# Kernel optimization log

Hardware: AMD Instinct MI355X
Metric: run time of the kernel (lower is better)

The kernel has to match this reference:

```python
import jax, jax.numpy as jnp
import numpy as np

B, L, N, H, HU = 512, 16, 10000, 128, 128

def _rn(k, shape, s=0.05):
    return jax.random.normal(k, shape, jnp.float32) * s

def setup_inputs():
    ks = jax.random.split(jax.random.key(0), 26)
    return dict(
        x=jax.random.normal(ks[0], (B, 2), jnp.float32),
        t0_res=jax.random.normal(ks[1], (B, 1), jnp.float32),
        node_inputs=jax.random.normal(ks[2], (B, 2 * L, N), jnp.float32),
        tau_inputs=jax.random.normal(ks[3], (B, L, 1), jnp.float32),
        end=jax.random.normal(ks[4], (B, 2), jnp.float32),
        coords=jax.random.normal(ks[5], (B, 2 * L, 2), jnp.float32),
        Wx1=_rn(ks[6], (1, 2)), Wx2=_rn(ks[7], (H, 1)), bx2=_rn(ks[8], (H,)),
        Wres=_rn(ks[9], (H, 1)), bres=_rn(ks[10], (H,)),
        Wnode=_rn(ks[11], (H, N)),
        Wtau=_rn(ks[12], (H, 1)), btau=_rn(ks[13], (H,)),
        Wend1=_rn(ks[14], (1, 2)), Wend2=_rn(ks[15], (H, 1)), bend2=_rn(ks[16], (H,)),
        Wcoord=_rn(ks[17], (H, 2)),
        lstm_Wih=_rn(ks[18], (7, 4 * H, H)), lstm_Whh=_rn(ks[19], (7, 4 * H, H)),
        lstm_bih=_rn(ks[20], (7, 4 * H)), lstm_bhh=_rn(ks[21], (7, 4 * H)),
        head_W1=_rn(ks[22], (7, HU, H)), head_b1=_rn(ks[23], (7, HU)),
        head_W2=_rn(ks[24], (7, 1, HU)), head_b2=_rn(ks[25], (7, 1)),
    )

def _lstm_last(s, Wih, Whh, bih, bhh):
    # s: [T, B, H] (time-first, like torch LSTM default). PyTorch gate order: i, f, g, o.
    h0 = jnp.zeros((s.shape[1], Whh.shape[1]), s.dtype)
    def step(carry, xt):
        h, c = carry
        g = xt @ Wih.T + h @ Whh.T + (bih + bhh)
        i, f, gg, o = jnp.split(g, 4, axis=-1)
        c = jax.nn.sigmoid(f) * c + jax.nn.sigmoid(i) * jnp.tanh(gg)
        h = jax.nn.sigmoid(o) * jnp.tanh(c)
        return (h, c), None
    (h, _), _ = jax.lax.scan(step, (h0, h0), s)
    return h  # last output == last hidden state

def _forward(x, t0_res, node_inputs, tau_inputs, end, coords,
             Wx1, Wx2, bx2, Wres, bres, Wnode, Wtau, btau,
             Wend1, Wend2, bend2, Wcoord,
             lstm_Wih, lstm_Whh, lstm_bih, lstm_bhh,
             head_W1, head_b1, head_W2, head_b2):
    xh = jnp.tanh((x @ Wx1.T) @ Wx2.T + bx2)        # [B,H]
    t0h = jnp.tanh(t0_res @ Wres.T + bres)          # [B,H]
    nodeh = node_inputs @ Wnode.T                   # [B,2L,H] (dominant memory-bound GEMM)
    tauh = jnp.tanh(tau_inputs @ Wtau.T + btau)     # [B,L,H]
    endh = (end @ Wend1.T) @ Wend2.T + bend2        # [B,H]
    coordh = coords @ Wcoord.T                      # [B,2L,H]
    ne, no = nodeh[:, 0::2], nodeh[:, 1::2]         # even/odd walk nodes [B,L,H]
    ce, co = coordh[:, 0::2], coordh[:, 1::2]
    def interleave(parts):  # k x [B,L,H] -> time-first [k*L, B, H], per-step order preserved
        s = jnp.stack(parts, axis=2)
        return jnp.swapaxes(s.reshape(s.shape[0], -1, s.shape[-1]), 0, 1)
    pre = jnp.stack([xh, t0h], axis=0)  # [2,B,H]
    suf = endh[None]                    # [1,B,H]
    seqs = [
        jnp.concatenate([pre, interleave([tauh, ne, ce, no, co]), suf], 0),  # all        T=5L+3
        jnp.concatenate([pre, interleave([tauh]), suf], 0),                  # time       T=L+3
        jnp.swapaxes(nodeh, 0, 1),                                           # node       T=2L
        jnp.swapaxes(coordh, 0, 1),                                          # coord      T=2L
        jnp.concatenate([pre, interleave([tauh, ne, no]), suf], 0),          # node_time  T=3L+3
        interleave([ne, ce, no, co]),                                        # node_coord T=4L
        jnp.concatenate([pre, interleave([tauh, ce, co]), suf], 0),          # time_coord T=3L+3
    ]
    outs = []
    for k, s in enumerate(seqs):
        h = _lstm_last(s, lstm_Wih[k], lstm_Whh[k], lstm_bih[k], lstm_bhh[k])
        outs.append(jnp.tanh(h @ head_W1[k].T + head_b1[k]) @ head_W2[k].T + head_b2[k])
    return tuple(outs)  # matches torch return order: all, time, node, coord, node_time, node_coord, time_coord

def reference(x, t0_res, node_inputs, tau_inputs, end, coords,
              Wx1, Wx2, bx2, Wres, bres, Wnode, Wtau, btau,
              Wend1, Wend2, bend2, Wcoord,
              lstm_Wih, lstm_Whh, lstm_bih, lstm_bhh,
              head_W1, head_b1, head_W2, head_b2):
    return _forward(x, t0_res, node_inputs, tau_inputs, end, coords,
                    Wx1, Wx2, bx2, Wres, bres, Wnode, Wtau, btau,
                    Wend1, Wend2, bend2, Wcoord,
                    lstm_Wih, lstm_Whh, lstm_bih, lstm_bhh,
                    head_W1, head_b1, head_W2, head_b2)
```

## Files before the change

kernel.cpp:

```cpp
#include <hip/hip_runtime.h>
#include <hip/hip_fp16.h>

typedef _Float16 f16;
typedef _Float16 f16x8 __attribute__((ext_vector_type(8)));
typedef float f32x4 __attribute__((ext_vector_type(4)));

#define NB 512
#define NL 16
#define NK 10000
#define NH 128
#define NSF 316
#define NT128 79

__device__ __forceinline__ float fast_exp2(float x) {
#if __has_builtin(__builtin_amdgcn_exp2f)
  return __builtin_amdgcn_exp2f(x);
#else
  return exp2f(x);
#endif
}
__device__ __forceinline__ float fast_rcp(float x) {
#if __has_builtin(__builtin_amdgcn_rcpf)
  return __builtin_amdgcn_rcpf(x);
#else
  return 1.f / x;
#endif
}
__device__ __forceinline__ float sigf(float x) {
  return fast_rcp(1.f + fast_exp2(-1.44269504f * x));
}
__device__ __forceinline__ float tanh_fast(float x) {
  return 2.f * fast_rcp(1.f + fast_exp2(-2.88539008f * x)) - 1.f;
}

__device__ __forceinline__ void gload16(const void* g, void* l) {
  __builtin_amdgcn_global_load_lds(
      (const __attribute__((address_space(1))) unsigned int*)g,
      (__attribute__((address_space(3))) unsigned int*)l, 16, 0, 0);
}

__global__ void prep_kernel(
    const float* __restrict__ x, const float* __restrict__ t0,
    const float* __restrict__ tau, const float* __restrict__ endi,
    const float* __restrict__ coords,
    const float* __restrict__ Wx1, const float* __restrict__ Wx2,
    const float* __restrict__ bx2, const float* __restrict__ Wres,
    const float* __restrict__ bres, const float* __restrict__ Wnode,
    const float* __restrict__ Wtau, const float* __restrict__ btau,
    const float* __restrict__ Wend1, const float* __restrict__ Wend2,
    const float* __restrict__ bend2, const float* __restrict__ Wcoord,
    const float* __restrict__ Wih, const float* __restrict__ Whh,
    const float* __restrict__ bih, const float* __restrict__ bhh,
    f16* __restrict__ xh, f16* __restrict__ t0h, f16* __restrict__ endh,
    f16* __restrict__ tauh, f16* __restrict__ coordh, f16* __restrict__ Wf,
    f16* __restrict__ Wih16, f16* __restrict__ Whh16, float* __restrict__ bsum) {
  const int tid0 = blockIdx.x * blockDim.x + threadIdx.x;
  const int stride = gridDim.x * blockDim.x;

  const int nWf = NSF * 4096;
  const int nW = 7 * 512 * NH;
  const int nb = 7 * 512;
  const int nxh = NB * NH;
  const int ntau = NB * NL * NH;
  const int nco = NB * 2 * NL * NH;

  for (int i = tid0; i < nWf; i += stride) {
    const int s = i >> 12, r = i & 4095;
    const int nt = r >> 9, l2 = r & 511;
    const int lane = l2 >> 3, e = l2 & 7;
    const int kg = lane >> 4, lr = lane & 15;
    const int col = nt * 16 + lr;
    const int k = s * 32 + kg * 8 + e;
    Wf[i] = (k < NK) ? (f16)Wnode[(size_t)col * NK + k] : (f16)0.f;
  }
  for (int i = tid0; i < nW; i += stride) {
    Wih16[i] = (f16)Wih[i];
    Whh16[i] = (f16)Whh[i];
  }
  for (int i = tid0; i < nb; i += stride) bsum[i] = bih[i] + bhh[i];
  for (int i = tid0; i < nxh; i += stride) {
    const int b = i >> 7, h = i & 127;
    const float s = x[2 * b] * Wx1[0] + x[2 * b + 1] * Wx1[1];
    xh[i] = (f16)tanhf(s * Wx2[h] + bx2[h]);
    t0h[i] = (f16)tanhf(t0[b] * Wres[h] + bres[h]);
    const float e = endi[2 * b] * Wend1[0] + endi[2 * b + 1] * Wend1[1];
    endh[i] = (f16)(e * Wend2[h] + bend2[h]);
  }
  for (int i = tid0; i < ntau; i += stride) {
    const int h = i & 127, bl = i >> 7;
    tauh[i] = (f16)tanhf(tau[bl] * Wtau[h] + btau[h]);
  }
  for (int i = tid0; i < nco; i += stride) {
    const int h = i & 127, br = i >> 7;
    coordh[i] = (f16)(coords[2 * br] * Wcoord[2 * h] +
                      coords[2 * br + 1] * Wcoord[2 * h + 1]);
  }
}

__global__ __launch_bounds__(512, 2) void node_gemm(const float* __restrict__ A,
                                                    const f16* __restrict__ Wf,
                                                    f16* __restrict__ Cn) {
  __shared__ char lds[4][32768];
  const int tid = threadIdx.x;
  const int w = tid >> 6, l = tid & 63;
  const int lr = l & 15, kg = l >> 4;
  const int r0 = blockIdx.x * 64;
  char* lds0 = &lds[0][0];

  const char* ap[4];
  int bnd[4];
#pragma unroll
  for (int i = 0; i < 4; i++) {
    const int row = w * 8 + i * 2 + (l >> 5);
    const int bswz = ((l & 31) * 16) ^ ((row & 7) << 4);
    ap[i] = (const char*)A + (size_t)(r0 + row) * 40000 + bswz;
    bnd[i] = 39984 - bswz;
  }

  const int rs = w & 3;
  const int nt0 = (w >> 2) * 4;
  int rdoA[4][2];
#pragma unroll
  for (int ks = 0; ks < 4; ks++) {
    const int row = rs * 16 + lr;
    const int s = (row & 7) << 4;
#pragma unroll
    for (int h = 0; h < 2; h++)
      rdoA[ks][h] = row * 512 + ((ks * 128 + kg * 32 + h * 16) ^ s);
  }

  f32x4 acc[4];
#pragma unroll
  for (int j = 0; j < 4; j++) {
    f32x4 z = {0.f, 0.f, 0.f, 0.f};
    acc[j] = z;
  }

  auto burst = [&](int ta) {
    const int tb0 = ta * 512, tb1 = tb0 + 512;
    char* d0 = lds0 + (ta & 3) * 32768 + w * 4096;
    char* d1 = lds0 + ((ta + 1) & 3) * 32768 + w * 4096;
    const bool two = (ta + 1 < NT128);
#pragma unroll
    for (int i = 0; i < 4; i++) {
      gload16(ap[i] + (tb0 < bnd[i] ? tb0 : bnd[i]), d0 + i * 1024);
      if (two) gload16(ap[i] + (tb1 < bnd[i] ? tb1 : bnd[i]), d1 + i * 1024);
    }
  };

  auto loadB = [&](int t, f16x8 (&B)[4][4]) {
    const f16* bp = Wf + (size_t)(4 * t) * 4096 + nt0 * 512 + l * 8;
#pragma unroll
    for (int j = 0; j < 4; j++)
#pragma unroll
      for (int ks = 0; ks < 4; ks++)
        B[j][ks] = *(const f16x8*)(bp + (size_t)ks * 4096 + j * 512);
  };

  auto compute = [&](int buf, const f16x8 (&B)[4][4]) {
    const char* cb = lds0 + buf * 32768;
#pragma unroll
    for (int ks = 0; ks < 4; ks++) {
      const f32x4 a0 = *(const f32x4*)(cb + rdoA[ks][0]);
      const f32x4 a1 = *(const f32x4*)(cb + rdoA[ks][1]);
      f16x8 af;
      af[0] = (f16)a0[0]; af[1] = (f16)a0[1]; af[2] = (f16)a0[2]; af[3] = (f16)a0[3];
      af[4] = (f16)a1[0]; af[5] = (f16)a1[1]; af[6] = (f16)a1[2]; af[7] = (f16)a1[3];
#pragma unroll
      for (int j = 0; j < 4; j++)
        acc[j] = __builtin_amdgcn_mfma_f32_16x16x32_f16(af, B[j][ks], acc[j], 0, 0, 0);
    }
  };

  f16x8 BA[4][4], BB[4][4];

  burst(0);
  loadB(0, BA);

  for (int e = 0; e < NT128; e += 2) {
    asm volatile("s_waitcnt vmcnt(16)" ::: "memory");
    __builtin_amdgcn_s_barrier();
    if (e + 1 < NT128) loadB(e + 1, BB);
    if (e + 2 < NT128) burst(e + 2);
    compute(e & 3, BA);
    if (e + 1 < NT128) {
      if (e + 2 < NT128) loadB(e + 2, BA);
      compute((e + 1) & 3, BB);
    }
  }

  f16* crow = Cn + (size_t)(r0 + rs * 16 + kg * 4) * NH + nt0 * 16 + lr;
#pragma unroll
  for (int j = 0; j < 4; j++)
#pragma unroll
    for (int jr = 0; jr < 4; jr++)
      crow[(size_t)jr * NH + j * 16] = (f16)acc[j][jr];
}

__global__ __launch_bounds__(512, 2) void lstm_run(
    const f16* __restrict__ xh, const f16* __restrict__ t0h,
    const f16* __restrict__ endh, const f16* __restrict__ tauh,
    const f16* __restrict__ nodeh, const f16* __restrict__ coordh,
    const f16* __restrict__ Wih16, const f16* __restrict__ Whh16,
    const float* __restrict__ bsum, const float* __restrict__ hW1,
    const float* __restrict__ hb1, const float* __restrict__ hW2,
    const float* __restrict__ hb2, float* __restrict__ out) {
  __shared__ f16 hbuf[2][16 * NH];
  __shared__ float hu[16 * NH];

  const int k = blockIdx.x >> 5;
  const int b0 = (blockIdx.x & 31) << 4;
  const int w = threadIdx.x >> 6;
  const int l = threadIdx.x & 63;
  const int lr = l & 15, kg = l >> 4;

  int len;
  switch (k) {
    case 0: len = 83; break;
    case 1: len = 19; break;
    case 2: len = 32; break;
    case 3: len = 32; break;
    case 4: len = 51; break;
    case 5: len = 64; break;
    default: len = 51; break;
  }

  auto xptr = [&](int t) -> const f16* {
    const f16* cb; int bstr, idx;
    if (k == 2) { cb = nodeh; bstr = 32 * NH; idx = t; }
    else if (k == 3) { cb = coordh; bstr = 32 * NH; idx = t; }
    else if (k == 5) {
      const int q = t >> 2, r = t & 3;
      cb = (r == 0 || r == 2) ? nodeh : coordh;
      bstr = 32 * NH;
      idx = 2 * q + ((r >= 2) ? 1 : 0);
    } else {
      if (t == 0) { cb = xh; bstr = NH; idx = 0; }
      else if (t == 1) { cb = t0h; bstr = NH; idx = 0; }
      else if (t == len - 1) { cb = endh; bstr = NH; idx = 0; }
      else {
        const int u = t - 2;
        if (k == 0) {
          const int q = u / 5, r = u - 5 * q;
          if (r == 0) { cb = tauh; bstr = 16 * NH; idx = q; }
          else if (r == 1) { cb = nodeh; bstr = 32 * NH; idx = 2 * q; }
          else if (r == 2) { cb = coordh; bstr = 32 * NH; idx = 2 * q; }
          else if (r == 3) { cb = nodeh; bstr = 32 * NH; idx = 2 * q + 1; }
          else { cb = coordh; bstr = 32 * NH; idx = 2 * q + 1; }
        } else if (k == 1) { cb = tauh; bstr = 16 * NH; idx = u; }
        else if (k == 4) {
          const int q = u / 3, r = u - 3 * q;
          if (r == 0) { cb = tauh; bstr = 16 * NH; idx = q; }
          else { cb = nodeh; bstr = 32 * NH; idx = 2 * q + (r - 1); }
        } else {
          const int q = u / 3, r = u - 3 * q;
          if (r == 0) { cb = tauh; bstr = 16 * NH; idx = q; }
          else { cb = coordh; bstr = 32 * NH; idx = 2 * q + (r - 1); }
        }
      }
    }
    return cb + (size_t)(b0 + lr) * bstr + idx * NH + kg * 8;
  };

  f16x8 Wh[4][4], Wi[4][4];
  float bias[4];
  {
    const f16* whb = Whh16 + (size_t)k * 512 * NH;
    const f16* wib = Wih16 + (size_t)k * 512 * NH;
#pragma unroll
    for (int g = 0; g < 4; g++) {
      const int col = g * 128 + w * 16 + lr;
      bias[g] = bsum[k * 512 + col];
#pragma unroll
      for (int kc = 0; kc < 4; kc++) {
        Wh[kc][g] = *(const f16x8*)(whb + (size_t)col * NH + kc * 32 + kg * 8);
        Wi[kc][g] = *(const f16x8*)(wib + (size_t)col * NH + kc * 32 + kg * 8);
      }
    }
  }

  char* lds0 = (char*)&hbuf[0][0];
  *(unsigned long long*)(lds0 + threadIdx.x * 8) = 0ull;
  __syncthreads();

  float c[4] = {0, 0, 0, 0};

  int rdo[4];
#pragma unroll
  for (int kc = 0; kc < 4; kc++) {
    const int colb = (kc * 32 + kg * 8) * 2;
    rdo[kc] = lr * 256 + (colb ^ ((lr & 7) << 4));
  }
  int wro[4];
#pragma unroll
  for (int jr = 0; jr < 4; jr++) {
    const int hrow = kg * 4 + jr;
    const int hcol = w * 16 + lr;
    wro[jr] = hrow * 256 + ((hcol * 2) ^ ((hrow & 7) << 4));
  }

  f16x8 axc[4];
  {
    const f16* xp = xptr(0);
#pragma unroll
    for (int kc = 0; kc < 4; kc++) axc[kc] = *(const f16x8*)(xp + kc * 32);
  }

  int cur = 0;
  for (int t = 0; t < len; t++) {
    char* rb = lds0 + cur * 4096;
    f16x8 ah[4];
#pragma unroll
    for (int kc = 0; kc < 4; kc++) ah[kc] = *(const f16x8*)(rb + rdo[kc]);

    f16x8 axn[4];
    if (t + 1 < len) {
      const f16* xp = xptr(t + 1);
#pragma unroll
      for (int kc = 0; kc < 4; kc++) axn[kc] = *(const f16x8*)(xp + kc * 32);
    }

    f32x4 acc[4];
#pragma unroll
    for (int g = 0; g < 4; g++) {
      f32x4 binit = {bias[g], bias[g], bias[g], bias[g]};
      acc[g] = binit;
    }
#pragma unroll
    for (int kc = 0; kc < 4; kc++)
#pragma unroll
      for (int g = 0; g < 4; g++)
        acc[g] = __builtin_amdgcn_mfma_f32_16x16x32_f16(axc[kc], Wi[kc][g], acc[g], 0, 0, 0);
#pragma unroll
    for (int kc = 0; kc < 4; kc++)
#pragma unroll
      for (int g = 0; g < 4; g++)
        acc[g] = __builtin_amdgcn_mfma_f32_16x16x32_f16(ah[kc], Wh[kc][g], acc[g], 0, 0, 0);

    char* wb = lds0 + (cur ^ 1) * 4096;
#pragma unroll
    for (int jr = 0; jr < 4; jr++) {
      const float iv = acc[0][jr];
      const float fv = acc[1][jr];
      const float gv = acc[2][jr];
      const float ov = acc[3][jr];
      const float cn = sigf(fv) * c[jr] + sigf(iv) * tanh_fast(gv);
      c[jr] = cn;
      const float hn = sigf(ov) * tanh_fast(cn);
      *(f16*)(wb + wro[jr]) = (f16)hn;
    }
    __syncthreads();
#pragma unroll
    for (int kc = 0; kc < 4; kc++) axc[kc] = axn[kc];
    cur ^= 1;
  }

  {
    char* rb = lds0 + cur * 4096;
    f16x8 ah[4];
#pragma unroll
    for (int kc = 0; kc < 4; kc++) ah[kc] = *(const f16x8*)(rb + rdo[kc]);
    const float* W1 = hW1 + (size_t)k * NH * NH;
    const int col = w * 16 + lr;
    f32x4 hacc;
    {
      const float b1 = hb1[k * NH + col];
      f32x4 binit = {b1, b1, b1, b1};
      hacc = binit;
    }
#pragma unroll
    for (int kc = 0; kc < 4; kc++) {
      const float* wrow = W1 + (size_t)col * NH + kc * 32 + kg * 8;
      const f32x4 w0 = *(const f32x4*)(wrow);
      const f32x4 w1 = *(const f32x4*)(wrow + 4);
      f16x8 wv;
      wv[0] = (f16)w0[0]; wv[1] = (f16)w0[1]; wv[2] = (f16)w0[2]; wv[3] = (f16)w0[3];
      wv[4] = (f16)w1[0]; wv[5] = (f16)w1[1]; wv[6] = (f16)w1[2]; wv[7] = (f16)w1[3];
      hacc = __builtin_amdgcn_mfma_f32_16x16x32_f16(ah[kc], wv, hacc, 0, 0, 0);
    }
#pragma unroll
    for (int jr = 0; jr < 4; jr++)
      hu[(kg * 4 + jr) * NH + col] = tanh_fast(hacc[jr]);
  }
  __syncthreads();
  if (w == 0) {
    const int b = l >> 2, part = l & 3;
    const float* W2 = hW2 + (size_t)k * NH;
    float s = 0.f;
#pragma unroll
    for (int j = 0; j < 32; j++)
      s += hu[b * NH + part * 32 + j] * W2[part * 32 + j];
    s += __shfl_xor(s, 1);
    s += __shfl_xor(s, 2);
    if (part == 0) out[k * NB + b0 + b] = s + hb2[k];
  }
}

extern "C" void kernel_launch(void* const* d_in, const int* in_sizes, int n_in,
                              void* d_out, int out_size, void* d_ws, size_t ws_size,
                              hipStream_t stream) {
  (void)in_sizes; (void)n_in; (void)out_size; (void)ws_size;
  const float* x = (const float*)d_in[0];
  const float* t0 = (const float*)d_in[1];
  const float* node = (const float*)d_in[2];
  const float* tau = (const float*)d_in[3];
  const float* endi = (const float*)d_in[4];
  const float* coords = (const float*)d_in[5];
  const float* Wx1 = (const float*)d_in[6];
  const float* Wx2 = (const float*)d_in[7];
  const float* bx2 = (const float*)d_in[8];
  const float* Wres = (const float*)d_in[9];
  const float* bres = (const float*)d_in[10];
  const float* Wnode = (const float*)d_in[11];
  const float* Wtau = (const float*)d_in[12];
  const float* btau = (const float*)d_in[13];
  const float* Wend1 = (const float*)d_in[14];
  const float* Wend2 = (const float*)d_in[15];
  const float* bend2 = (const float*)d_in[16];
  const float* Wcoord = (const float*)d_in[17];
  const float* Wih = (const float*)d_in[18];
  const float* Whh = (const float*)d_in[19];
  const float* bih = (const float*)d_in[20];
  const float* bhh = (const float*)d_in[21];
  const float* hW1 = (const float*)d_in[22];
  const float* hb1 = (const float*)d_in[23];
  const float* hW2 = (const float*)d_in[24];
  const float* hb2 = (const float*)d_in[25];

  char* ws = (char*)d_ws;
  f16* xh = (f16*)ws;      ws += (size_t)NB * NH * 2;
  f16* t0h = (f16*)ws;     ws += (size_t)NB * NH * 2;
  f16* endh = (f16*)ws;    ws += (size_t)NB * NH * 2;
  f16* tauh = (f16*)ws;    ws += (size_t)NB * NL * NH * 2;
  f16* nodeh = (f16*)ws;   ws += (size_t)NB * 2 * NL * NH * 2;
  f16* coordh = (f16*)ws;  ws += (size_t)NB * 2 * NL * NH * 2;
  f16* Wf = (f16*)ws;      ws += (size_t)NSF * 4096 * 2;
  f16* Wih16 = (f16*)ws;   ws += (size_t)7 * 512 * NH * 2;
  f16* Whh16 = (f16*)ws;   ws += (size_t)7 * 512 * NH * 2;
  float* bsum = (float*)ws;

  prep_kernel<<<1024, 256, 0, stream>>>(
      x, t0, tau, endi, coords, Wx1, Wx2, bx2, Wres, bres, Wnode, Wtau, btau,
      Wend1, Wend2, bend2, Wcoord, Wih, Whh, bih, bhh,
      xh, t0h, endh, tauh, coordh, Wf, Wih16, Whh16, bsum);
  node_gemm<<<256, 512, 0, stream>>>(node, Wf, nodeh);
  lstm_run<<<224, 512, 0, stream>>>(xh, t0h, endh, tauh, nodeh, coordh,
                                    Wih16, Whh16, bsum, hW1, hb1, hW2, hb2,
                                    (float*)d_out);
}
```

Before: 299.3 us.

## Retile node GEMM warps to 64x32 split-K with LDS reduction

The node-projection GEMM changes its per-warp tile. Before, each warp covered 16 rows by 64 columns over the full K slice. Now each warp covers all 64 rows by 32 columns over half of each K tile, and the two K halves are summed through LDS at the end. This cuts per-warp weight (B) fragment loads from global memory by 4x and shrinks the B register buffers. In exchange, each warp does more LDS reads of A and more fp32-to-fp16 conversions, and an extra LDS reduction plus barrier is added. The vmcnt wait is retuned to the smaller load count and the last tile is peeled out of the loop.

```diff
diff --git a/kernel.cpp b/kernel.cpp
--- a/kernel.cpp
+++ b/kernel.cpp
@@ -117,24 +117,29 @@
     bnd[i] = 39984 - bswz;
   }
 
-  const int rs = w & 3;
-  const int nt0 = (w >> 2) * 4;
-  int rdoA[4][2];
-#pragma unroll
-  for (int ks = 0; ks < 4; ks++) {
-    const int row = rs * 16 + lr;
+  const int cp = w >> 1;
+  const int kw = w & 1;
+  int rdoA[4][2][2];
+#pragma unroll
+  for (int rg = 0; rg < 4; rg++) {
+    const int row = rg * 16 + lr;
     const int s = (row & 7) << 4;
 #pragma unroll
-    for (int h = 0; h < 2; h++)
-      rdoA[ks][h] = row * 512 + ((ks * 128 + kg * 32 + h * 16) ^ s);
-  }
-
-  f32x4 acc[4];
-#pragma unroll
-  for (int j = 0; j < 4; j++) {
-    f32x4 z = {0.f, 0.f, 0.f, 0.f};
-    acc[j] = z;
-  }
+    for (int ks = 0; ks < 2; ks++)
+#pragma unroll
+      for (int h = 0; h < 2; h++)
+        rdoA[rg][ks][h] =
+            row * 512 + ((kw * 256 + ks * 128 + kg * 32 + h * 16) ^ s);
+  }
+
+  f32x4 acc[4][2];
+#pragma unroll
+  for (int rg = 0; rg < 4; rg++)
+#pragma unroll
+    for (int j = 0; j < 2; j++) {
+      f32x4 z = {0.f, 0.f, 0.f, 0.f};
+      acc[rg][j] = z;
+    }
 
   auto burst = [&](int ta) {
     const int tb0 = ta * 512, tb1 = tb0 + 512;
@@ -148,53 +153,77 @@
     }
   };
 
-  auto loadB = [&](int t, f16x8 (&B)[4][4]) {
-    const f16* bp = Wf + (size_t)(4 * t) * 4096 + nt0 * 512 + l * 8;
-#pragma unroll
-    for (int j = 0; j < 4; j++)
-#pragma unroll
-      for (int ks = 0; ks < 4; ks++)
+  auto loadB = [&](int t, f16x8 (&B)[2][2]) {
+    const f16* bp = Wf + (size_t)(4 * t + 2 * kw) * 4096 + cp * 1024 + l * 8;
+#pragma unroll
+    for (int j = 0; j < 2; j++)
+#pragma unroll
+      for (int ks = 0; ks < 2; ks++)
         B[j][ks] = *(const f16x8*)(bp + (size_t)ks * 4096 + j * 512);
   };
 
-  auto compute = [&](int buf, const f16x8 (&B)[4][4]) {
-    const char* cb = lds0 + buf * 32768;
-#pragma unroll
-    for (int ks = 0; ks < 4; ks++) {
-      const f32x4 a0 = *(const f32x4*)(cb + rdoA[ks][0]);
-      const f32x4 a1 = *(const f32x4*)(cb + rdoA[ks][1]);
-      f16x8 af;
-      af[0] = (f16)a0[0]; af[1] = (f16)a0[1]; af[2] = (f16)a0[2]; af[3] = (f16)a0[3];
-      af[4] = (f16)a1[0]; af[5] = (f16)a1[1]; af[6] = (f16)a1[2]; af[7] = (f16)a1[3];
-#pragma unroll
-      for (int j = 0; j < 4; j++)
-        acc[j] = __builtin_amdgcn_mfma_f32_16x16x32_f16(af, B[j][ks], acc[j], 0, 0, 0);
-    }
+  auto compute = [&](int t, const f16x8 (&B)[2][2]) {
+    const char* cb = lds0 + (t & 3) * 32768;
+#pragma unroll
+    for (int ks = 0; ks < 2; ks++)
+#pragma unroll
+      for (int rg = 0; rg < 4; rg++) {
+        const f32x4 a0 = *(const f32x4*)(cb + rdoA[rg][ks][0]);
+        const f32x4 a1 = *(const f32x4*)(cb + rdoA[rg][ks][1]);
+        f16x8 af;
+        af[0] = (f16)a0[0]; af[1] = (f16)a0[1];
+        af[2] = (f16)a0[2]; af[3] = (f16)a0[3];
+        af[4] = (f16)a1[0]; af[5] = (f16)a1[1];
+        af[6] = (f16)a1[2]; af[7] = (f16)a1[3];
+#pragma unroll
+        for (int j = 0; j < 2; j++)
+          acc[rg][j] =
+              __builtin_amdgcn_mfma_f32_16x16x32_f16(af, B[j][ks], acc[rg][j], 0, 0, 0);
+      }
   };
 
-  f16x8 BA[4][4], BB[4][4];
+  f16x8 BA[2][2], BB[2][2];
 
   burst(0);
   loadB(0, BA);
 
-  for (int e = 0; e < NT128; e += 2) {
-    asm volatile("s_waitcnt vmcnt(16)" ::: "memory");
+  for (int e = 0; e < NT128 - 1; e += 2) {
+    asm volatile("s_waitcnt vmcnt(4)" ::: "memory");
     __builtin_amdgcn_s_barrier();
-    if (e + 1 < NT128) loadB(e + 1, BB);
-    if (e + 2 < NT128) burst(e + 2);
-    compute(e & 3, BA);
-    if (e + 1 < NT128) {
-      if (e + 2 < NT128) loadB(e + 2, BA);
-      compute((e + 1) & 3, BB);
-    }
-  }
-
-  f16* crow = Cn + (size_t)(r0 + rs * 16 + kg * 4) * NH + nt0 * 16 + lr;
-#pragma unroll
-  for (int j = 0; j < 4; j++)
-#pragma unroll
-    for (int jr = 0; jr < 4; jr++)
-      crow[(size_t)jr * NH + j * 16] = (f16)acc[j][jr];
+    loadB(e + 1, BB);
+    burst(e + 2);
+    compute(e, BA);
+    loadB(e + 2, BA);
+    compute(e + 1, BB);
+  }
+  asm volatile("s_waitcnt vmcnt(0)" ::: "memory");
+  __builtin_amdgcn_s_barrier();
+  compute(78, BA);
+
+  if (kw == 1) {
+#pragma unroll
+    for (int rg = 0; rg < 4; rg++)
+#pragma unroll
+      for (int j = 0; j < 2; j++) {
+        const int tl = (cp * 4 + rg) * 2 + j;
+        *(f32x4*)(lds0 + tl * 1024 + l * 16) = acc[rg][j];
+      }
+  }
+  __syncthreads();
+  if (kw == 0) {
+#pragma unroll
+    for (int rg = 0; rg < 4; rg++)
+#pragma unroll
+      for (int j = 0; j < 2; j++) {
+        const int tl = (cp * 4 + rg) * 2 + j;
+        const f32x4 p = *(const f32x4*)(lds0 + tl * 1024 + l * 16);
+        const f32x4 s = acc[rg][j] + p;
+        f16* crow =
+            Cn + (size_t)(r0 + rg * 16 + kg * 4) * NH + cp * 32 + j * 16 + lr;
+#pragma unroll
+        for (int jr = 0; jr < 4; jr++) crow[(size_t)jr * NH] = (f16)s[jr];
+      }
+  }
 }
 
 __global__ __launch_bounds__(512, 2) void lstm_run(
```

Result: faster. 266.9 us (-10.8%).

## Halve node GEMM row tile to 32 rows and double grid for more CTAs

Applied to the files above, without the earlier changes.

The node projection GEMM now gives each block 32 rows instead of 64, launching 512 blocks instead of 256. LDS per block halves and launch bounds allow four blocks per CU. Each wave now covers a 16x32 output slice instead of 16x64. The loop tail is peeled so the last tile is computed after a full wait, which removes the per-iteration bound checks. The aim is to fill all CUs (256 blocks underfilled the 256-CU part at two per CU) and keep more loads in flight. In exchange, each block re-reads the full weight matrix from global memory, doubling total B traffic.

```diff
diff --git a/kernel.cpp b/kernel.cpp
--- a/kernel.cpp
+++ b/kernel.cpp
@@ -97,101 +97,106 @@
   }
 }
 
-__global__ __launch_bounds__(512, 2) void node_gemm(const float* __restrict__ A,
+__global__ __launch_bounds__(512, 4) void node_gemm(const float* __restrict__ A,
                                                     const f16* __restrict__ Wf,
                                                     f16* __restrict__ Cn) {
-  __shared__ char lds[4][32768];
+  __shared__ char lds[4][16384];
   const int tid = threadIdx.x;
   const int w = tid >> 6, l = tid & 63;
   const int lr = l & 15, kg = l >> 4;
-  const int r0 = blockIdx.x * 64;
+  const int r0 = blockIdx.x * 32;
   char* lds0 = &lds[0][0];
 
-  const char* ap[4];
-  int bnd[4];
-#pragma unroll
-  for (int i = 0; i < 4; i++) {
-    const int row = w * 8 + i * 2 + (l >> 5);
+  const char* ap[2];
+  int bnd[2];
+#pragma unroll
+  for (int i = 0; i < 2; i++) {
+    const int row = w * 4 + i * 2 + (l >> 5);
     const int bswz = ((l & 31) * 16) ^ ((row & 7) << 4);
     ap[i] = (const char*)A + (size_t)(r0 + row) * 40000 + bswz;
     bnd[i] = 39984 - bswz;
   }
 
-  const int rs = w & 3;
-  const int nt0 = (w >> 2) * 4;
+  const int rh = w & 1;
+  const int cq = w >> 1;
   int rdoA[4][2];
-#pragma unroll
-  for (int ks = 0; ks < 4; ks++) {
-    const int row = rs * 16 + lr;
+  {
+    const int row = rh * 16 + lr;
     const int s = (row & 7) << 4;
 #pragma unroll
-    for (int h = 0; h < 2; h++)
-      rdoA[ks][h] = row * 512 + ((ks * 128 + kg * 32 + h * 16) ^ s);
-  }
-
-  f32x4 acc[4];
-#pragma unroll
-  for (int j = 0; j < 4; j++) {
+    for (int ks = 0; ks < 4; ks++)
+#pragma unroll
+      for (int h = 0; h < 2; h++)
+        rdoA[ks][h] = row * 512 + ((ks * 128 + kg * 32 + h * 16) ^ s);
+  }
+
+  f32x4 acc[2];
+#pragma unroll
+  for (int j = 0; j < 2; j++) {
     f32x4 z = {0.f, 0.f, 0.f, 0.f};
     acc[j] = z;
   }
 
   auto burst = [&](int ta) {
     const int tb0 = ta * 512, tb1 = tb0 + 512;
-    char* d0 = lds0 + (ta & 3) * 32768 + w * 4096;
-    char* d1 = lds0 + ((ta + 1) & 3) * 32768 + w * 4096;
+    char* d0 = lds0 + (ta & 3) * 16384 + w * 2048;
+    char* d1 = lds0 + ((ta + 1) & 3) * 16384 + w * 2048;
     const bool two = (ta + 1 < NT128);
 #pragma unroll
-    for (int i = 0; i < 4; i++) {
+    for (int i = 0; i < 2; i++) {
       gload16(ap[i] + (tb0 < bnd[i] ? tb0 : bnd[i]), d0 + i * 1024);
       if (two) gload16(ap[i] + (tb1 < bnd[i] ? tb1 : bnd[i]), d1 + i * 1024);
     }
   };
 
-  auto loadB = [&](int t, f16x8 (&B)[4][4]) {
-    const f16* bp = Wf + (size_t)(4 * t) * 4096 + nt0 * 512 + l * 8;
-#pragma unroll
-    for (int j = 0; j < 4; j++)
+  auto loadB = [&](int t, f16x8 (&B)[2][4]) {
+    const f16* bp = Wf + (size_t)(4 * t) * 4096 + cq * 1024 + l * 8;
+#pragma unroll
+    for (int j = 0; j < 2; j++)
 #pragma unroll
       for (int ks = 0; ks < 4; ks++)
         B[j][ks] = *(const f16x8*)(bp + (size_t)ks * 4096 + j * 512);
   };
 
-  auto compute = [&](int buf, const f16x8 (&B)[4][4]) {
-    const char* cb = lds0 + buf * 32768;
+  auto compute = [&](int t, const f16x8 (&B)[2][4]) {
+    const char* cb = lds0 + (t & 3) * 16384;
 #pragma unroll
     for (int ks = 0; ks < 4; ks++) {
       const f32x4 a0 = *(const f32x4*)(cb + rdoA[ks][0]);
       const f32x4 a1 = *(const f32x4*)(cb + rdoA[ks][1]);
       f16x8 af;
-      af[0] = (f16)a0[0]; af[1] = (f16)a0[1]; af[2] = (f16)a0[2]; af[3] = (f16)a0[3];
-      af[4] = (f16)a1[0]; af[5] = (f16)a1[1]; af[6] = (f16)a1[2]; af[7] = (f16)a1[3];
-#pragma unroll
-      for (int j = 0; j < 4; j++)
-        acc[j] = __builtin_amdgcn_mfma_f32_16x16x32_f16(af, B[j][ks], acc[j], 0, 0, 0);
+      af[0] = (f16)a0[0]; af[1] = (f16)a0[1];
+      af[2] = (f16)a0[2]; af[3] = (f16)a0[3];
+      af[4] = (f16)a1[0]; af[5] = (f16)a1[1];
+      af[6] = (f16)a1[2]; af[7] = (f16)a1[3];
+#pragma unroll
+      for (int j = 0; j < 2; j++)
+        acc[j] =
+            __builtin_amdgcn_mfma_f32_16x16x32_f16(af, B[j][ks], acc[j], 0, 0, 0);
     }
   };
 
-  f16x8 BA[4][4], BB[4][4];
+  f16x8 BA[2][4], BB[2][4];
 
   burst(0);
   loadB(0, BA);
 
-  for (int e = 0; e < NT128; e += 2) {
-    asm volatile("s_waitcnt vmcnt(16)" ::: "memory");
+  for (int e = 0; e < NT128 - 1; e += 2) {
+    asm volatile("s_waitcnt vmcnt(8)" ::: "memory");
     __builtin_amdgcn_s_barrier();
-    if (e + 1 < NT128) loadB(e + 1, BB);
-    if (e + 2 < NT128) burst(e + 2);
-    compute(e & 3, BA);
-    if (e + 1 < NT128) {
-      if (e + 2 < NT128) loadB(e + 2, BA);
-      compute((e + 1) & 3, BB);
-    }
-  }
-
-  f16* crow = Cn + (size_t)(r0 + rs * 16 + kg * 4) * NH + nt0 * 16 + lr;
-#pragma unroll
-  for (int j = 0; j < 4; j++)
+    loadB(e + 1, BB);
+    burst(e + 2);
+    compute(e, BA);
+    loadB(e + 2, BA);
+    compute(e + 1, BB);
+  }
+  asm volatile("s_waitcnt vmcnt(0)" ::: "memory");
+  __builtin_amdgcn_s_barrier();
+  compute(78, BA);
+
+  f16* crow = Cn + (size_t)(r0 + rh * 16 + kg * 4) * NH + cq * 32 + lr;
+#pragma unroll
+  for (int j = 0; j < 2; j++)
 #pragma unroll
     for (int jr = 0; jr < 4; jr++)
       crow[(size_t)jr * NH + j * 16] = (f16)acc[j][jr];
@@ -443,7 +448,7 @@
       x, t0, tau, endi, coords, Wx1, Wx2, bx2, Wres, bres, Wnode, Wtau, btau,
       Wend1, Wend2, bend2, Wcoord, Wih, Whh, bih, bhh,
       xh, t0h, endh, tauh, coordh, Wf, Wih16, Whh16, bsum);
-  node_gemm<<<256, 512, 0, stream>>>(node, Wf, nodeh);
+  node_gemm<<<512, 512, 0, stream>>>(node, Wf, nodeh);
   lstm_run<<<224, 512, 0, stream>>>(xh, t0h, endh, tauh, nodeh, coordh,
                                     Wih16, Whh16, bsum, hW1, hb1, hW2, hb2,
                                     (float*)d_out);
```

Result: no change. 300.8 us (+0.5%).
